# Kernel tuning notes

Measured on AMD Instinct MI355X. Metric: run time of the kernel, lower is better.

## Reference

```python
import jax, jax.numpy as jnp
import numpy as np

TAG_SIZE = 64
START = 62  # tag_2_index[START_TAG]
END = 63    # tag_2_index[END_TAG]
NEG = -10000.0
L, B = 512, 1024


def setup_inputs() -> dict:
    key = jax.random.key(0)
    k1, k2, k3 = jax.random.split(key, 3)
    feats = jax.random.normal(k1, (L, B, TAG_SIZE), dtype=jnp.float32)
    tags = jax.random.randint(k2, (L, B), 0, 62)
    mask = jnp.ones((L, B), dtype=jnp.float32)
    transition = jax.random.normal(k3, (TAG_SIZE, TAG_SIZE), dtype=jnp.float32)
    # reset_parameters: never transition into START, never transition out of END
    transition = transition.at[START, :].set(NEG).at[:, END].set(NEG)
    return {"feats": feats, "tags": tags, "mask": mask, "transition": transition}


def _forward_allpath(feats, mask, transition):
    # feats: (L, B, T), mask: (L, B), transition: (T, T)
    Bsz, T = feats.shape[1], feats.shape[2]
    alpha0 = jnp.full((Bsz, T), NEG, feats.dtype).at[:, START].set(0.0)

    def step(alpha, xs):
        feat, m = xs  # feat: (B, T), m: (B,)
        # (B, next_tag, prev_tag)
        s = alpha[:, None, :] + transition[None, :, :] + feat[:, :, None]
        new = jax.nn.logsumexp(s, axis=-1)  # (B, T)
        alpha = new * m[:, None] + alpha * (1.0 - m[:, None])
        return alpha, None

    alpha, _ = jax.lax.scan(step, alpha0, (feats, mask))
    alpha = alpha + transition[END][None, :]
    return jax.nn.logsumexp(alpha, axis=-1)  # (B,)


def _score_realpath(feats, tags, mask, transition):
    Lh, Bsz, T = feats.shape
    tags_ext = jnp.concatenate(
        [jnp.full((1, Bsz), START, tags.dtype), tags], axis=0)  # (L+1, B)
    # emission score of the gold tag at each step: (L, B)
    emit = jnp.take_along_axis(feats, tags_ext[1:][:, :, None], axis=2)[..., 0]
    # transition[next_tag, prev_tag]: (L, B)
    trans = transition[tags_ext[1:], tags_ext[:-1]]
    scores = jnp.sum((emit + trans) * mask, axis=0)  # (B,)
    lengths = mask.sum(axis=0).astype(jnp.int32)  # (B,)
    last_tag = tags_ext[lengths, jnp.arange(Bsz)]  # tag at position len (START offset)
    return scores + transition[END, last_tag]


def reference(feats, tags, mask, transition):
    # CRF negative log-likelihood components: (allpath - realpath) per sample
    allpath = _forward_allpath(feats, mask, transition)
    realpath = _score_realpath(feats, tags, mask, transition)
    return allpath - realpath
```

## Files before the change

kernel.cpp:

```cpp
#include <hip/hip_runtime.h>

constexpr int TAGS = 64;
constexpr int START_T = 62;
constexpr int END_T = 63;
constexpr float NEGF = -10000.0f;
constexpr int L_DIM = 512;
constexpr int B_DIM = 1024;

__device__ __forceinline__ float lane_bcast(float x, int lane) {
    return __int_as_float(__builtin_amdgcn_readlane(__float_as_int(x), lane));
}

__device__ __forceinline__ float wave_max64(float x) {
#pragma unroll
    for (int off = 32; off >= 1; off >>= 1)
        x = fmaxf(x, __shfl_xor(x, off, 64));
    return x;
}

__device__ __forceinline__ float wave_sum64(float x) {
#pragma unroll
    for (int off = 32; off >= 1; off >>= 1)
        x += __shfl_xor(x, off, 64);
    return x;
}

__global__ __launch_bounds__(256, 1) void crf_fused(
    const float* __restrict__ feats,
    const int* __restrict__ tags,
    const float* __restrict__ mask,
    const float* __restrict__ trans,
    float* __restrict__ out)
{
    __shared__ float sE[TAGS][TAGS + 1];
    const int lane = threadIdx.x;
    const int wid  = threadIdx.y;
    const int b    = blockIdx.x * 4 + wid;
    const int tid  = wid * 64 + lane;

#pragma unroll
    for (int k = 0; k < (TAGS * TAGS) / 256; ++k) {
        int idx = tid + 256 * k;
        sE[idx >> 6][idx & 63] = expf(trans[idx]);
    }
    __syncthreads();

    float Erow[TAGS];
#pragma unroll
    for (int j = 0; j < TAGS; ++j) Erow[j] = sE[lane][j];
#pragma unroll
    for (int j = 0; j < TAGS; ++j) asm volatile("" : "+v"(Erow[j]));

    float a = (lane == START_T) ? 0.0f : NEGF;
    float M = 0.0f;

    const float* fptr = feats + (size_t)b * TAGS + lane;
    const size_t fstride = (size_t)B_DIM * TAGS;
    const float* mptr = mask + b;

    float f0 = fptr[0];
    float f1 = fptr[fstride];
    float m0 = mptr[0];
    float m1 = mptr[B_DIM];

#pragma unroll 2
    for (int l = 0; l < L_DIM; ++l) {
        float f2 = (l + 2 < L_DIM) ? fptr[(size_t)(l + 2) * fstride] : 0.0f;
        float m2 = (l + 2 < L_DIM) ? mptr[(size_t)(l + 2) * B_DIM] : 0.0f;

        float v = __expf(a - M);

        float a0 = 0.f, a1 = 0.f, a2 = 0.f, a3 = 0.f;
#pragma unroll
        for (int j = 0; j < TAGS; j += 4) {
            a0 = fmaf(Erow[j + 0], lane_bcast(v, j + 0), a0);
            a1 = fmaf(Erow[j + 1], lane_bcast(v, j + 1), a1);
            a2 = fmaf(Erow[j + 2], lane_bcast(v, j + 2), a2);
            a3 = fmaf(Erow[j + 3], lane_bcast(v, j + 3), a3);
        }
        float ssum = (a0 + a1) + (a2 + a3);

        float na = f0 + M + __logf(ssum);
        na = fmaxf(na, -1e30f);
        a = na * m0 + a * (1.0f - m0);

        M = lane_bcast(a, 0);

        f0 = f1; f1 = f2;
        m0 = m1; m1 = m2;
    }

    float x = a + trans[END_T * TAGS + lane];
    float Mx = wave_max64(x);
    float ex = __expf(x - Mx);
    float S = wave_sum64(ex);
    float allp = Mx + __logf(S);

    float sc = 0.0f, lensum = 0.0f;
#pragma unroll
    for (int k = 0; k < L_DIM / 64; ++k) {
        int l = lane + 64 * k;
        int tg = tags[l * B_DIM + b];
        int pv = (l == 0) ? START_T : tags[(l - 1) * B_DIM + b];
        float m = mask[l * B_DIM + b];
        float emit = feats[((size_t)l * B_DIM + b) * TAGS + tg];
        float tr = trans[tg * TAGS + pv];
        sc += (emit + tr) * m;
        lensum += m;
    }
    sc = wave_sum64(sc);
    lensum = wave_sum64(lensum);
    int len = (int)lensum;
    int last_tag = (len == 0) ? START_T : tags[(len - 1) * B_DIM + b];
    float realp = sc + trans[END_T * TAGS + last_tag];

    if (lane == 0) out[b] = allp - realp;
}

extern "C" void kernel_launch(void* const* d_in, const int* in_sizes, int n_in,
                              void* d_out, int out_size, void* d_ws, size_t ws_size,
                              hipStream_t stream) {
    const float* feats = (const float*)d_in[0];
    const int*   tags  = (const int*)d_in[1];
    const float* mask  = (const float*)d_in[2];
    const float* trans = (const float*)d_in[3];
    float* out = (float*)d_out;

    dim3 block(64, 4, 1);
    dim3 grid(B_DIM / 4, 1, 1);
    hipLaunchKernelGGL(crf_fused, grid, block, 0, stream,
                       feats, tags, mask, trans, out);
}
```

Measured before the change: 406.3 us.

## Broadcast alpha through LDS and use packed FMA with one wave per block

Replaces the 64 per-step readlane broadcasts with one LDS write of v and sixteen 128-bit LDS vector reads per step. The dot product now uses v_pk_fma_f32 on pairs, halving the FMA instruction count. The launch changes to one 64-thread block per batch element, which lets the per-step __syncthreads act on a single wave. The cost is an LDS round trip and a barrier on the serial recurrence critical path, and the inner loop is no longer unrolled.

```diff
diff --git a/kernel.cpp b/kernel.cpp
--- a/kernel.cpp
+++ b/kernel.cpp
@@ -6,6 +6,9 @@
 constexpr float NEGF = -10000.0f;
 constexpr int L_DIM = 512;
 constexpr int B_DIM = 1024;
+
+typedef float v2f __attribute__((ext_vector_type(2)));
+typedef float v4f __attribute__((ext_vector_type(4)));
 
 __device__ __forceinline__ float lane_bcast(float x, int lane) {
     return __int_as_float(__builtin_amdgcn_readlane(__float_as_int(x), lane));
@@ -25,31 +28,34 @@
     return x;
 }
 
-__global__ __launch_bounds__(256, 1) void crf_fused(
+__device__ __forceinline__ void pk_fma(v2f& acc, v2f e, v2f v) {
+    asm volatile("v_pk_fma_f32 %0, %1, %2, %0" : "+v"(acc) : "v"(e), "v"(v));
+}
+
+__global__ __attribute__((amdgpu_waves_per_eu(1))) __launch_bounds__(64)
+void crf_fused(
     const float* __restrict__ feats,
     const int* __restrict__ tags,
     const float* __restrict__ mask,
     const float* __restrict__ trans,
     float* __restrict__ out)
 {
-    __shared__ float sE[TAGS][TAGS + 1];
+    __shared__ float sE[TAGS][TAGS + 2];
+    __shared__ __align__(16) float vbuf[2][TAGS];
     const int lane = threadIdx.x;
-    const int wid  = threadIdx.y;
-    const int b    = blockIdx.x * 4 + wid;
-    const int tid  = wid * 64 + lane;
+    const int b    = blockIdx.x;
 
 #pragma unroll
-    for (int k = 0; k < (TAGS * TAGS) / 256; ++k) {
-        int idx = tid + 256 * k;
-        sE[idx >> 6][idx & 63] = expf(trans[idx]);
-    }
+    for (int k = 0; k < TAGS; ++k)
+        sE[k][lane] = expf(trans[k * TAGS + lane]);
     __syncthreads();
 
-    float Erow[TAGS];
+    v2f Erow[TAGS / 2];
 #pragma unroll
-    for (int j = 0; j < TAGS; ++j) Erow[j] = sE[lane][j];
+    for (int j = 0; j < TAGS / 2; ++j)
+        Erow[j] = *(const v2f*)&sE[lane][2 * j];
 #pragma unroll
-    for (int j = 0; j < TAGS; ++j) asm volatile("" : "+v"(Erow[j]));
+    for (int j = 0; j < TAGS / 2; ++j) asm volatile("" : "+v"(Erow[j]));
 
     float a = (lane == START_T) ? 0.0f : NEGF;
     float M = 0.0f;
@@ -63,22 +69,31 @@
     float m0 = mptr[0];
     float m1 = mptr[B_DIM];
 
-#pragma unroll 2
+#pragma unroll 1
     for (int l = 0; l < L_DIM; ++l) {
         float f2 = (l + 2 < L_DIM) ? fptr[(size_t)(l + 2) * fstride] : 0.0f;
         float m2 = (l + 2 < L_DIM) ? mptr[(size_t)(l + 2) * B_DIM] : 0.0f;
 
         float v = __expf(a - M);
+        float* vb = vbuf[l & 1];
+        vb[lane] = v;
+        __syncthreads();
 
-        float a0 = 0.f, a1 = 0.f, a2 = 0.f, a3 = 0.f;
+        v2f acc0 = {0.f, 0.f}, acc1 = {0.f, 0.f};
+        v2f acc2 = {0.f, 0.f}, acc3 = {0.f, 0.f};
 #pragma unroll
-        for (int j = 0; j < TAGS; j += 4) {
-            a0 = fmaf(Erow[j + 0], lane_bcast(v, j + 0), a0);
-            a1 = fmaf(Erow[j + 1], lane_bcast(v, j + 1), a1);
-            a2 = fmaf(Erow[j + 2], lane_bcast(v, j + 2), a2);
-            a3 = fmaf(Erow[j + 3], lane_bcast(v, j + 3), a3);
+        for (int k = 0; k < TAGS / 4; ++k) {
+            v4f vv = *(const v4f*)&vb[4 * k];
+            if (k & 1) {
+                pk_fma(acc2, Erow[2 * k],     vv.lo);
+                pk_fma(acc3, Erow[2 * k + 1], vv.hi);
+            } else {
+                pk_fma(acc0, Erow[2 * k],     vv.lo);
+                pk_fma(acc1, Erow[2 * k + 1], vv.hi);
+            }
         }
-        float ssum = (a0 + a1) + (a2 + a3);
+        v2f t = (acc0 + acc1) + (acc2 + acc3);
+        float ssum = t.x + t.y;
 
         float na = f0 + M + __logf(ssum);
         na = fmaxf(na, -1e30f);
@@ -126,8 +141,8 @@
     const float* trans = (const float*)d_in[3];
     float* out = (float*)d_out;
 
-    dim3 block(64, 4, 1);
-    dim3 grid(B_DIM / 4, 1, 1);
+    dim3 block(64, 1, 1);
+    dim3 grid(B_DIM, 1, 1);
     hipLaunchKernelGGL(crf_fused, grid, block, 0, stream,
                        feats, tags, mask, trans, out);
 }
```

Measured after the change: 623.9 us. +53.6%, slower.
